# Performance work log

Measured on AMD Instinct MI355X. Metric: run time of the kernel, lower is better.

Reference implementation:

```python
import jax, jax.numpy as jnp
import numpy as np

N_NODES = 40000
N_EDGES = 640000
C = 128        # in_channels == hidden_channels
H = 8          # heads
D = C // H     # head dim = 16
L = 2          # num HGTConv layers
OUT = 64       # final fc out_channels


def _segment_softmax(logits, seg, num_segments):
    # logits: [E, H], seg: [E] destination ids
    m = jax.ops.segment_max(logits, seg, num_segments=num_segments)
    m = jnp.where(jnp.isfinite(m), m, 0.0)  # empty segments -> 0
    e = jnp.exp(logits - m[seg])
    s = jax.ops.segment_sum(e, seg, num_segments=num_segments)
    return e / (s[seg] + 1e-16)


def setup_inputs() -> dict:
    key = jax.random.key(0)
    ks = jax.random.split(key, 20)
    p = lambda k, shape, s=0.05: (jax.random.normal(k, shape, jnp.float32) * s)
    x = jax.random.normal(ks[0], (N_NODES, C), jnp.float32)
    edge_index = jax.random.randint(ks[1], (2, N_EDGES), 0, N_NODES, jnp.int64)
    return {
        "x": x,
        "edge_index": edge_index,
        # per-layer stacked params (all layers have C->C dims)
        "Wk": p(ks[2], (L, C, C)), "bk": jnp.zeros((L, C), jnp.float32),
        "Wq": p(ks[3], (L, C, C)), "bq": jnp.zeros((L, C), jnp.float32),
        "Wv": p(ks[4], (L, C, C)), "bv": jnp.zeros((L, C), jnp.float32),
        "a_rel": p(ks[5], (L, H, D, D), 0.1),  # relation key transform
        "m_rel": p(ks[6], (L, H, D, D), 0.1),  # relation message transform
        "p_rel": jnp.ones((L, H), jnp.float32),  # relation prior per head
        "skip": jnp.ones((L,), jnp.float32),      # skip gate logits
        "aW": p(ks[7], (L, C, C)), "ab": jnp.zeros((L, C), jnp.float32),
        "fcW": p(ks[8], (C, OUT)), "fcb": jnp.zeros((OUT,), jnp.float32),
    }


def reference(x, edge_index, Wk, bk, Wq, bq, Wv, bv, a_rel, m_rel, p_rel, skip,
              aW, ab, fcW, fcb):
    src, dst = edge_index[0], edge_index[1]
    n = x.shape[0]
    n_layers, heads, d = a_rel.shape[0], a_rel.shape[1], a_rel.shape[2]
    inv_sqrt_d = 1.0 / np.sqrt(d).astype(np.float32)

    h = x
    for l in range(n_layers):
        k = (h @ Wk[l] + bk[l]).reshape(n, heads, d)
        q = (h @ Wq[l] + bq[l]).reshape(n, heads, d)
        v = (h @ Wv[l] + bv[l]).reshape(n, heads, d)
        # relation-specific transforms applied at node level (single edge type)
        k2 = jnp.einsum('nhd,hde->nhe', k, a_rel[l])
        v2 = jnp.einsum('nhd,hde->nhe', v, m_rel[l])
        # per-edge attention logits [E, H]
        logits = jnp.sum(q[dst] * k2[src], axis=-1) * p_rel[l] * inv_sqrt_d
        alpha = _segment_softmax(logits, dst, n)                 # [E, H]
        msg = v2[src] * alpha[:, :, None]                        # [E, H, D]
        agg = jax.ops.segment_sum(msg, dst, num_segments=n)      # [N, H, D]
        agg = agg.reshape(n, heads * d)
        a = jax.nn.gelu(agg) @ aW[l] + ab[l]
        beta = jax.nn.sigmoid(skip[l])
        h = beta * a + (1.0 - beta) * h     # HGT skip (dims match)
        h = jax.nn.relu(h)                  # model-level relu
    return h @ fcW + fcb
```

## Files before the change

kernel.cpp:

```cpp
#include <hip/hip_runtime.h>
#include <hip/hip_bf16.h>
#include <math.h>

#define NN 40000
#define NE 640000

typedef __attribute__((ext_vector_type(8))) short short8;
typedef __attribute__((ext_vector_type(8))) unsigned short u16x8;
typedef __attribute__((ext_vector_type(4))) float f32x4;
typedef __attribute__((ext_vector_type(2))) float f32v2;
typedef _Float16 h16x2 __attribute__((ext_vector_type(2)));

#define WBLOCKS 547
#define GBLOCKS 625
#define NCO 157
#define P1B 160
#define EPB 4000
#define BCAP 5120

#if __has_builtin(__builtin_amdgcn_cvt_pk_f32_fp8) && __has_builtin(__builtin_amdgcn_cvt_pk_fp8_f32)
#define HAS_FP8CVT 1
#else
#define HAS_FP8CVT 0
#endif

__device__ __forceinline__ float fast_exp2(float x) {
#if __has_builtin(__builtin_amdgcn_exp2f)
    return __builtin_amdgcn_exp2f(x);
#else
    return exp2f(x);
#endif
}

__device__ __forceinline__ float gelu_tanh(float x) {
    float x3 = x * x * x;
    float u = 0.7978845608028654f * (x + 0.044715f * x3);
    float t = 1.0f - 2.0f / (1.0f + fast_exp2(2.885390081777927f * u));
    return 0.5f * x * (1.0f + t);
}

__device__ __forceinline__ unsigned short f2bf(float v) {
    __hip_bfloat16 h = __float2bfloat16(v);
    return *reinterpret_cast<unsigned short*>(&h);
}

__device__ __forceinline__ unsigned short f2h(float v) {
    union { _Float16 h; unsigned short u; } c;
    c.h = (_Float16)v;
    return c.u;
}

__device__ __forceinline__ float bf2f(unsigned short u) {
    union { unsigned int i; float f; } c;
    c.i = ((unsigned int)u) << 16;
    return c.f;
}

#if HAS_FP8CVT
__device__ __forceinline__ unsigned int f32x4_to_fp8(float a, float b, float c, float d) {
    int r = 0;
    r = __builtin_amdgcn_cvt_pk_fp8_f32(a, b, r, false);
    r = __builtin_amdgcn_cvt_pk_fp8_f32(c, d, r, true);
    return (unsigned int)r;
}
__device__ __forceinline__ void fp8x4_to_f32(unsigned int w, float* o) {
    f32v2 lo = __builtin_amdgcn_cvt_pk_f32_fp8((int)w, false);
    f32v2 hi = __builtin_amdgcn_cvt_pk_f32_fp8((int)w, true);
    o[0] = lo[0]; o[1] = lo[1]; o[2] = hi[0]; o[3] = hi[1];
}
#else
__device__ __forceinline__ unsigned char f2fp8_sw(float x) {
    union { float f; unsigned u; } c; c.f = x;
    unsigned sgn = (c.u >> 31) << 7;
    c.u &= 0x7fffffffu;
    if (!(c.f < 464.f)) return (unsigned char)(sgn | 0x7e);
    if (c.f < 0.0009765625f) return (unsigned char)sgn;
    if (c.f < 0.015625f) {
        int q = (int)rintf(c.f * 512.f);
        if (q > 7) return (unsigned char)(sgn | 0x08);
        return (unsigned char)(sgn | q);
    }
    unsigned u = c.u;
    unsigned lsb = (u >> 20) & 1;
    u += 0x7ffffu + lsb;
    int e8 = (int)(u >> 23) - 127 + 7;
    if (e8 > 15) return (unsigned char)(sgn | 0x7e);
    unsigned m = (u >> 20) & 7;
    return (unsigned char)(sgn | (e8 << 3) | m);
}
__device__ __forceinline__ float fp8_to_f32_sw(unsigned char b) {
    int e = (b >> 3) & 15, m = b & 7;
    float v = (e == 0) ? ldexpf((float)m, -9) : ldexpf(8.0f + (float)m, e - 10);
    return (b & 0x80) ? -v : v;
}
__device__ __forceinline__ unsigned int f32x4_to_fp8(float a, float b, float c, float d) {
    return (unsigned int)f2fp8_sw(a) | ((unsigned int)f2fp8_sw(b) << 8) |
           ((unsigned int)f2fp8_sw(c) << 16) | ((unsigned int)f2fp8_sw(d) << 24);
}
__device__ __forceinline__ void fp8x4_to_f32(unsigned int w, float* o) {
    o[0] = fp8_to_f32_sw((unsigned char)(w & 0xff));
    o[1] = fp8_to_f32_sw((unsigned char)((w >> 8) & 0xff));
    o[2] = fp8_to_f32_sw((unsigned char)((w >> 16) & 0xff));
    o[3] = fp8_to_f32_sw((unsigned char)((w >> 24) & 0xff));
}
#endif

union kv8 { u16x8 u; h16x2 p[4]; _Float16 h[8]; };
union frag8 { short8 s; unsigned short u[8]; u16x8 v; };

__global__ __launch_bounds__(256) void prep_kernel(
    const float* __restrict__ Wq, const float* __restrict__ bq,
    const float* __restrict__ Wk, const float* __restrict__ bk,
    const float* __restrict__ a_rel,
    const float* __restrict__ Wv, const float* __restrict__ bv,
    const float* __restrict__ m_rel,
    const float* __restrict__ p_rel,
    const float* __restrict__ aW, const float* __restrict__ fcW,
    unsigned short* __restrict__ BfT, float* __restrict__ biasf,
    unsigned short* __restrict__ aWT, unsigned short* __restrict__ fcWT,
    const int* __restrict__ eidx, int* __restrict__ gcur, int* __restrict__ ebuk)
{
    if (blockIdx.x < P1B) {
        __shared__ int cnt[NCO];
        __shared__ int cur[NCO];
        int b = blockIdx.x;
        int t = threadIdx.x;
        if (t < NCO) cnt[t] = 0;
        __syncthreads();
        int bs = b * EPB;
        for (int e = bs + t; e < bs + EPB; e += 256)
            atomicAdd(&cnt[eidx[NE + e] >> 8], 1);
        __syncthreads();
        if (t < NCO) cur[t] = atomicAdd(&gcur[t], cnt[t]);
        __syncthreads();
        for (int e = bs + t; e < bs + EPB; e += 256) {
            int s = eidx[e];
            int d = eidx[NE + e];
            int cb = d >> 8;
            int pos = atomicAdd(&cur[cb], 1);
            ebuk[cb * BCAP + pos] = ((d & 255) << 16) | s;
        }
        return;
    }
    int idx = (blockIdx.x - P1B) * 256 + threadIdx.x;
    if (idx < 2 * 129 * 384) {
        int l = idx / (129 * 384);
        int j = idx - l * (129 * 384);
        int r = j / 384;
        int col = j - r * 384;
        const float* Wq_l = Wq + l * 16384;
        const float* Wk_l = Wk + l * 16384;
        const float* Wv_l = Wv + l * 16384;
        const float* ar_l = a_rel + l * 2048;
        const float* mr_l = m_rel + l * 2048;
        float val;
        if (col < 128) {
            val = (r < 128) ? Wq_l[r * 128 + col] : bq[l * 128 + col];
        } else if (col < 256) {
            int cc = col - 128; int h = cc >> 4; int eo = cc & 15;
            float scale = p_rel[l * 8 + h] * 0.25f * 1.4426950408889634f;
            float s = 0.f;
            #pragma unroll
            for (int d = 0; d < 16; ++d) {
                float w = (r < 128) ? Wk_l[r * 128 + h * 16 + d] : bk[l * 128 + h * 16 + d];
                s += w * ar_l[h * 256 + d * 16 + eo];
            }
            val = s * scale;
        } else {
            int cc = col - 256; int h = cc >> 4; int eo = cc & 15;
            float s = 0.f;
            #pragma unroll
            for (int d = 0; d < 16; ++d) {
                float w = (r < 128) ? Wv_l[r * 128 + h * 16 + d] : bv[l * 128 + h * 16 + d];
                s += w * mr_l[h * 256 + d * 16 + eo];
            }
            val = s;
        }
        if (r < 128) BfT[(size_t)l * 49152 + (size_t)col * 128 + r] = f2bf(val);
        else         biasf[l * 384 + col] = val;
    } else if (idx < 2 * 129 * 384 + 2 * 16384) {
        int i = idx - 2 * 129 * 384;
        int l = i >> 14; int j = i & 16383;
        int r = j >> 7, c = j & 127;
        aWT[(size_t)l * 16384 + (size_t)c * 128 + r] = f2bf(aW[(size_t)l * 16384 + r * 128 + c]);
    } else {
        int i = idx - (2 * 129 * 384 + 2 * 16384);
        int c = i >> 7, r = i & 127;
        fcWT[(size_t)c * 128 + r] = f2bf(fcW[(size_t)r * 64 + c]);
    }
}

__global__ __launch_bounds__(256) void qkv0_p3_kernel(
    const float* __restrict__ Af, const unsigned short* __restrict__ BT,
    const float* __restrict__ bias,
    unsigned short* __restrict__ qb, unsigned char* __restrict__ kvb,
    const int* __restrict__ gcnt, const int* __restrict__ ebuk,
    int* __restrict__ deg, int* __restrict__ offs, int* __restrict__ srcSorted)
{
    if (blockIdx.x >= GBLOCKS) {
        __shared__ int hist[256], loffs[256], cur[256];
        int c = blockIdx.x - GBLOCKS;
        int t = threadIdx.x;
        int base = c * BCAP;
        int end = base + gcnt[c];
        hist[t] = 0;
        __syncthreads();
        for (int i = base + t; i < end; i += 256)
            atomicAdd(&hist[ebuk[i] >> 16], 1);
        __syncthreads();
        int v = hist[t];
        loffs[t] = v;
        __syncthreads();
        #pragma unroll
        for (int off = 1; off < 256; off <<= 1) {
            int u = (t >= off) ? loffs[t - off] : 0;
            __syncthreads();
            loffs[t] += u;
            __syncthreads();
        }
        int excl = loffs[t] - v;
        int n = c * 256 + t;
        if (n < NN) { deg[n] = v; offs[n] = base + excl; }
        cur[t] = excl;
        __syncthreads();
        for (int i = base + t; i < end; i += 256) {
            int p = ebuk[i];
            int pos = atomicAdd(&cur[p >> 16], 1);
            srcSorted[base + pos] = p & 0xffff;
        }
        return;
    }
    __shared__ unsigned short Bs[64][136];
    int t = threadIdx.x;
    int row0 = blockIdx.x * 64;
    int w = t >> 6;
    int lr = t & 15;
    int quad = (t & 63) >> 4;
    int row = row0 + w * 16 + lr;

    frag8 af[4];
    {
        const float* ap = Af + (size_t)row * 128 + quad * 8;
        #pragma unroll
        for (int kc = 0; kc < 4; ++kc) {
            float4 a0 = *(const float4*)(ap + kc * 32);
            float4 a1 = *(const float4*)(ap + kc * 32 + 4);
            af[kc].u[0] = f2bf(a0.x); af[kc].u[1] = f2bf(a0.y);
            af[kc].u[2] = f2bf(a0.z); af[kc].u[3] = f2bf(a0.w);
            af[kc].u[4] = f2bf(a1.x); af[kc].u[5] = f2bf(a1.y);
            af[kc].u[6] = f2bf(a1.z); af[kc].u[7] = f2bf(a1.w);
        }
    }

    #pragma unroll
    for (int ct = 0; ct < 6; ++ct) {
        if (ct) __syncthreads();
        #pragma unroll
        for (int i = 0; i < 4; ++i) {
            int idx = t + i * 256;
            int r = idx >> 4;
            int c8 = (idx & 15) * 8;
            *(u16x8*)(&Bs[r][c8]) = *(const u16x8*)(BT + (size_t)(ct * 64 + r) * 128 + c8);
        }
        __syncthreads();
        f32x4 acc[4] = {{0.f,0.f,0.f,0.f},{0.f,0.f,0.f,0.f},
                        {0.f,0.f,0.f,0.f},{0.f,0.f,0.f,0.f}};
        #pragma unroll
        for (int kc = 0; kc < 4; ++kc) {
            #pragma unroll
            for (int n4 = 0; n4 < 4; ++n4) {
                short8 bfr = *(const short8*)(&Bs[n4 * 16 + lr][kc * 32 + quad * 8]);
                acc[n4] = __builtin_amdgcn_mfma_f32_16x16x32_bf16(bfr, af[kc].s, acc[n4], 0, 0, 0);
            }
        }
        if (ct < 2) {
            unsigned short* dst = qb + (size_t)row * 128 + ct * 64;
            #pragma unroll
            for (int n4 = 0; n4 < 4; ++n4) {
                int colb = n4 * 16 + quad * 4;
                float4 bv = *(const float4*)(bias + ct * 64 + colb);
                ushort4 o;
                o.x = f2h(acc[n4][0] + bv.x);
                o.y = f2h(acc[n4][1] + bv.y);
                o.z = f2h(acc[n4][2] + bv.z);
                o.w = f2h(acc[n4][3] + bv.w);
                *(ushort4*)(dst + colb) = o;
            }
        } else {
            unsigned char* dst = kvb + (size_t)row * 256 + (ct - 2) * 64;
            #pragma unroll
            for (int n4 = 0; n4 < 4; ++n4) {
                int colb = n4 * 16 + quad * 4;
                float4 bv = *(const float4*)(bias + ct * 64 + colb);
                *(unsigned int*)(dst + colb) = f32x4_to_fp8(
                    acc[n4][0] + bv.x, acc[n4][1] + bv.y,
                    acc[n4][2] + bv.z, acc[n4][3] + bv.w);
            }
        }
    }
}

template <int HPFMT, int P2>
__global__ __launch_bounds__(256) void fused_kernel(
    const unsigned short* __restrict__ aggb,
    const unsigned short* __restrict__ aWT, const float* __restrict__ ab,
    const float* __restrict__ skip_p,
    const float* __restrict__ HprevF, const unsigned short* __restrict__ HprevB,
    unsigned short* __restrict__ hb_out,
    const unsigned short* __restrict__ W2T, const float* __restrict__ bias2,
    unsigned short* __restrict__ qb, unsigned char* __restrict__ kvb,
    float* __restrict__ outF)
{
    __shared__ unsigned short As[64][136];
    __shared__ unsigned short Bs[64][136];
    int t = threadIdx.x;
    int row0 = blockIdx.x * 64;
    int w = t >> 6;
    int lr = t & 15;
    int quad = (t & 63) >> 4;
    int row = row0 + w * 16 + lr;

    frag8 agf[4];
    {
        const unsigned short* ap = aggb + (size_t)row * 128 + quad * 8;
        #pragma unroll
        for (int kc = 0; kc < 4; ++kc) {
            u16x8 u = *(const u16x8*)(ap + kc * 32);
            #pragma unroll
            for (int j = 0; j < 8; ++j) agf[kc].u[j] = f2bf(gelu_tanh(bf2f(u[j])));
        }
    }

    float sv = skip_p[0];
    float beta = 1.f / (1.f + expf(-sv));
    float omb = 1.f - beta;

    f32x4 hacc[2][4];
    #pragma unroll
    for (int ct = 0; ct < 2; ++ct) {
        if (ct) __syncthreads();
        #pragma unroll
        for (int i = 0; i < 4; ++i) {
            int idx = t + i * 256;
            int r = idx >> 4;
            int c8 = (idx & 15) * 8;
            *(u16x8*)(&Bs[r][c8]) = *(const u16x8*)(aWT + (size_t)(ct * 64 + r) * 128 + c8);
        }
        __syncthreads();
        #pragma unroll
        for (int n4 = 0; n4 < 4; ++n4) hacc[ct][n4] = (f32x4){0.f,0.f,0.f,0.f};
        #pragma unroll
        for (int kc = 0; kc < 4; ++kc) {
            #pragma unroll
            for (int n4 = 0; n4 < 4; ++n4) {
                short8 bfr = *(const short8*)(&Bs[n4 * 16 + lr][kc * 32 + quad * 8]);
                hacc[ct][n4] = __builtin_amdgcn_mfma_f32_16x16x32_bf16(bfr, agf[kc].s, hacc[ct][n4], 0, 0, 0);
            }
        }
    }

    #pragma unroll
    for (int ct = 0; ct < 2; ++ct) {
        #pragma unroll
        for (int n4 = 0; n4 < 4; ++n4) {
            int colb = ct * 64 + n4 * 16 + quad * 4;
            float4 bv = *(const float4*)(ab + colb);
            float hp[4];
            if (HPFMT == 0) {
                float4 h4 = *(const float4*)(HprevF + (size_t)row * 128 + colb);
                hp[0] = h4.x; hp[1] = h4.y; hp[2] = h4.z; hp[3] = h4.w;
            } else {
                ushort4 h4 = *(const ushort4*)(HprevB + (size_t)row * 128 + colb);
                hp[0] = bf2f(h4.x); hp[1] = bf2f(h4.y); hp[2] = bf2f(h4.z); hp[3] = bf2f(h4.w);
            }
            ushort4 o;
            o.x = f2bf(fmaxf(beta * (hacc[ct][n4][0] + bv.x) + omb * hp[0], 0.f));
            o.y = f2bf(fmaxf(beta * (hacc[ct][n4][1] + bv.y) + omb * hp[1], 0.f));
            o.z = f2bf(fmaxf(beta * (hacc[ct][n4][2] + bv.z) + omb * hp[2], 0.f));
            o.w = f2bf(fmaxf(beta * (hacc[ct][n4][3] + bv.w) + omb * hp[3], 0.f));
            *(ushort4*)(&As[w * 16 + lr][colb]) = o;
            if (P2 == 0) *(ushort4*)(hb_out + (size_t)row * 128 + colb) = o;
        }
    }
    __syncthreads();

    if (P2 == 0) {
        #pragma unroll
        for (int ct = 0; ct < 6; ++ct) {
            if (ct) __syncthreads();
            #pragma unroll
            for (int i = 0; i < 4; ++i) {
                int idx = t + i * 256;
                int r = idx >> 4;
                int c8 = (idx & 15) * 8;
                *(u16x8*)(&Bs[r][c8]) = *(const u16x8*)(W2T + (size_t)(ct * 64 + r) * 128 + c8);
            }
            __syncthreads();
            f32x4 acc[4] = {{0.f,0.f,0.f,0.f},{0.f,0.f,0.f,0.f},
                            {0.f,0.f,0.f,0.f},{0.f,0.f,0.f,0.f}};
            #pragma unroll
            for (int kc = 0; kc < 4; ++kc) {
                short8 afr = *(const short8*)(&As[w * 16 + lr][kc * 32 + quad * 8]);
                #pragma unroll
                for (int n4 = 0; n4 < 4; ++n4) {
                    short8 bfr = *(const short8*)(&Bs[n4 * 16 + lr][kc * 32 + quad * 8]);
                    acc[n4] = __builtin_amdgcn_mfma_f32_16x16x32_bf16(bfr, afr, acc[n4], 0, 0, 0);
                }
            }
            if (ct < 2) {
                unsigned short* dst = qb + (size_t)row * 128 + ct * 64;
                #pragma unroll
                for (int n4 = 0; n4 < 4; ++n4) {
                    int colb = n4 * 16 + quad * 4;
                    float4 bv = *(const float4*)(bias2 + ct * 64 + colb);
                    ushort4 o;
                    o.x = f2h(acc[n4][0] + bv.x);
                    o.y = f2h(acc[n4][1] + bv.y);
                    o.z = f2h(acc[n4][2] + bv.z);
                    o.w = f2h(acc[n4][3] + bv.w);
                    *(ushort4*)(dst + colb) = o;
                }
            } else {
                unsigned char* dst = kvb + (size_t)row * 256 + (ct - 2) * 64;
                #pragma unroll
                for (int n4 = 0; n4 < 4; ++n4) {
                    int colb = n4 * 16 + quad * 4;
                    float4 bv = *(const float4*)(bias2 + ct * 64 + colb);
                    *(unsigned int*)(dst + colb) = f32x4_to_fp8(
                        acc[n4][0] + bv.x, acc[n4][1] + bv.y,
                        acc[n4][2] + bv.z, acc[n4][3] + bv.w);
                }
            }
        }
    } else {
        #pragma unroll
        for (int i = 0; i < 4; ++i) {
            int idx = t + i * 256;
            int r = idx >> 4;
            int c8 = (idx & 15) * 8;
            *(u16x8*)(&Bs[r][c8]) = *(const u16x8*)(W2T + (size_t)r * 128 + c8);
        }
        __syncthreads();
        f32x4 acc[4] = {{0.f,0.f,0.f,0.f},{0.f,0.f,0.f,0.f},
                        {0.f,0.f,0.f,0.f},{0.f,0.f,0.f,0.f}};
        #pragma unroll
        for (int kc = 0; kc < 4; ++kc) {
            short8 afr = *(const short8*)(&As[w * 16 + lr][kc * 32 + quad * 8]);
            #pragma unroll
            for (int n4 = 0; n4 < 4; ++n4) {
                short8 bfr = *(const short8*)(&Bs[n4 * 16 + lr][kc * 32 + quad * 8]);
                acc[n4] = __builtin_amdgcn_mfma_f32_16x16x32_bf16(bfr, afr, acc[n4], 0, 0, 0);
            }
        }
        #pragma unroll
        for (int n4 = 0; n4 < 4; ++n4) {
            int colb = n4 * 16 + quad * 4;
            float4 bv = *(const float4*)(bias2 + colb);
            float4 o;
            o.x = acc[n4][0] + bv.x;
            o.y = acc[n4][1] + bv.y;
            o.z = acc[n4][2] + bv.z;
            o.w = acc[n4][3] + bv.w;
            *(float4*)(outF + (size_t)row * 64 + colb) = o;
        }
    }
}

__global__ __launch_bounds__(256) void aggregate_kernel(
    const unsigned short* __restrict__ qb, const unsigned char* __restrict__ kvb,
    const int* __restrict__ deg, const int* __restrict__ offs,
    const int* __restrict__ srcSorted, unsigned short* __restrict__ aggb)
{
    int n = (blockIdx.x * 256 + threadIdx.x) >> 6;
    int lane = threadIdx.x & 63;
    int es = lane >> 3;
    int h = lane & 7;

    float qf[16];
    {
        kv8 a, b;
        a.u = *(const u16x8*)(qb + (size_t)n * 128 + h * 16);
        b.u = *(const u16x8*)(qb + (size_t)n * 128 + h * 16 + 8);
        #pragma unroll
        for (int j = 0; j < 8; ++j) { qf[j] = (float)a.h[j]; qf[8 + j] = (float)b.h[j]; }
    }
    float acc[16];
    #pragma unroll
    for (int j = 0; j < 16; ++j) acc[j] = 0.f;
    float den = 0.f;

    int start = offs[n];
    int d = deg[n];
    if (d > 0) {
        int ng = (d + 7) >> 3;
        int lastIdx = start + d - 1;

        int4 kA, vA, kB, vB;
        {
            int i0 = start + es; if (i0 > lastIdx) i0 = lastIdx;
            const unsigned char* p = kvb + (size_t)srcSorted[i0] * 256 + h * 16;
            kA = *(const int4*)p;
            vA = *(const int4*)(p + 128);
        }
        kB = kA; vB = vA;
        if (ng > 1) {
            int i1 = start + 8 + es; if (i1 > lastIdx) i1 = lastIdx;
            const unsigned char* p = kvb + (size_t)srcSorted[i1] * 256 + h * 16;
            kB = *(const int4*)p;
            vB = *(const int4*)(p + 128);
        }

        for (int g = 0; g < ng; ++g) {
            int4 kC = kA, vC = vA;
            if (g + 2 < ng) {
                int ni = start + (g + 2) * 8 + es; if (ni > lastIdx) ni = lastIdx;
                const unsigned char* p = kvb + (size_t)srcSorted[ni] * 256 + h * 16;
                kC = *(const int4*)p;
                vC = *(const int4*)(p + 128);
            }
            float pdot = 0.f;
            {
                float kf[16];
                fp8x4_to_f32((unsigned int)kA.x, kf);
                fp8x4_to_f32((unsigned int)kA.y, kf + 4);
                fp8x4_to_f32((unsigned int)kA.z, kf + 8);
                fp8x4_to_f32((unsigned int)kA.w, kf + 12);
                #pragma unroll
                for (int j = 0; j < 16; ++j) pdot = fmaf(kf[j], qf[j], pdot);
            }
            float ev = (g * 8 + es < d) ? fast_exp2(pdot) : 0.f;
            den += ev;
            {
                float vf[16];
                fp8x4_to_f32((unsigned int)vA.x, vf);
                fp8x4_to_f32((unsigned int)vA.y, vf + 4);
                fp8x4_to_f32((unsigned int)vA.z, vf + 8);
                fp8x4_to_f32((unsigned int)vA.w, vf + 12);
                #pragma unroll
                for (int j = 0; j < 16; ++j) acc[j] = fmaf(vf[j], ev, acc[j]);
            }
            kA = kB; vA = vB;
            kB = kC; vB = vC;
        }
    }
    #pragma unroll
    for (int m = 8; m < 64; m <<= 1) {
        den += __shfl_xor(den, m, 64);
        #pragma unroll
        for (int j = 0; j < 16; ++j) acc[j] += __shfl_xor(acc[j], m, 64);
    }
    if (es == 0) {
        float w = 1.f / (den + 1e-16f);
        u16x8 o0, o1;
        #pragma unroll
        for (int j = 0; j < 8; ++j) {
            o0[j] = f2bf(acc[j] * w);
            o1[j] = f2bf(acc[j + 8] * w);
        }
        *(u16x8*)(aggb + (size_t)n * 128 + h * 16) = o0;
        *(u16x8*)(aggb + (size_t)n * 128 + h * 16 + 8) = o1;
    }
}

extern "C" void kernel_launch(void* const* d_in, const int* in_sizes, int n_in,
                              void* d_out, int out_size, void* d_ws, size_t ws_size,
                              hipStream_t stream) {
    const float* x     = (const float*)d_in[0];
    const int*   eidx  = (const int*)d_in[1];
    const float* Wk    = (const float*)d_in[2];
    const float* bk    = (const float*)d_in[3];
    const float* Wq    = (const float*)d_in[4];
    const float* bq    = (const float*)d_in[5];
    const float* Wv    = (const float*)d_in[6];
    const float* bv    = (const float*)d_in[7];
    const float* a_rel = (const float*)d_in[8];
    const float* m_rel = (const float*)d_in[9];
    const float* p_rel = (const float*)d_in[10];
    const float* skip  = (const float*)d_in[11];
    const float* aW    = (const float*)d_in[12];
    const float* ab    = (const float*)d_in[13];
    const float* fcW   = (const float*)d_in[14];
    const float* fcb   = (const float*)d_in[15];
    float* out = (float*)d_out;

    float* biasf = (float*)d_ws;
    unsigned short* hb   = (unsigned short*)(biasf + 768);
    unsigned short* qb   = hb + (size_t)NN * 128;
    unsigned char*  kvb  = (unsigned char*)(qb + (size_t)NN * 128);
    unsigned short* aggb = (unsigned short*)(kvb + (size_t)NN * 256);
    unsigned short* BfT  = aggb + (size_t)NN * 128;
    unsigned short* aWT  = BfT + 2 * 384 * 128;
    unsigned short* fcWT = aWT + 2 * 128 * 128;
    int* deg       = (int*)(fcWT + 64 * 128);
    int* offs      = deg + NN;
    int* gcur      = offs + NN;
    int* ebuk      = gcur + 160;
    int* srcSorted = ebuk + NCO * BCAP;

    hipMemsetAsync(gcur, 0, NCO * sizeof(int), stream);

    prep_kernel<<<P1B + WBLOCKS, 256, 0, stream>>>(
        Wq, bq, Wk, bk, a_rel, Wv, bv, m_rel, p_rel, aW, fcW,
        BfT, biasf, aWT, fcWT, eidx, gcur, ebuk);

    qkv0_p3_kernel<<<GBLOCKS + NCO, 256, 0, stream>>>(
        x, BfT, biasf, qb, kvb, gcur, ebuk, deg, offs, srcSorted);
    aggregate_kernel<<<NN / 4, 256, 0, stream>>>(qb, kvb, deg, offs, srcSorted, aggb);

    fused_kernel<0, 0><<<GBLOCKS, 256, 0, stream>>>(
        aggb, aWT, ab, skip, x, nullptr, hb,
        BfT + 49152, biasf + 384, qb, kvb, nullptr);
    aggregate_kernel<<<NN / 4, 256, 0, stream>>>(qb, kvb, deg, offs, srcSorted, aggb);

    fused_kernel<1, 2><<<GBLOCKS, 256, 0, stream>>>(
        aggb, aWT + 16384, ab + 128, skip + 1, nullptr, hb, nullptr,
        fcWT, fcb, nullptr, nullptr, out);
}
```

Measured before the change: 240.1 us.

## Fuse edge aggregation into the per-layer GEMM kernel via shared memory

```diff
diff --git a/kernel.cpp b/kernel.cpp
--- a/kernel.cpp
+++ b/kernel.cpp
@@ -195,7 +195,7 @@
     const float* __restrict__ bias,
     unsigned short* __restrict__ qb, unsigned char* __restrict__ kvb,
     const int* __restrict__ gcnt, const int* __restrict__ ebuk,
-    int* __restrict__ deg, int* __restrict__ offs, int* __restrict__ srcSorted)
+    int* __restrict__ podeg, int* __restrict__ srcSorted)
 {
     if (blockIdx.x >= GBLOCKS) {
         __shared__ int hist[256], loffs[256], cur[256];
@@ -220,7 +220,7 @@
         }
         int excl = loffs[t] - v;
         int n = c * 256 + t;
-        if (n < NN) { deg[n] = v; offs[n] = base + excl; }
+        if (n < NN) podeg[n] = (base + excl) | (v << 20);
         cur[t] = excl;
         __syncthreads();
         for (int i = base + t; i < end; i += 256) {
@@ -301,14 +301,15 @@
 }
 
 template <int HPFMT, int P2>
-__global__ __launch_bounds__(256) void fused_kernel(
-    const unsigned short* __restrict__ aggb,
+__global__ __launch_bounds__(256) void merged_kernel(
+    const unsigned short* __restrict__ qb, const unsigned char* __restrict__ kvb,
+    const int* __restrict__ podeg, const int* __restrict__ srcSorted,
     const unsigned short* __restrict__ aWT, const float* __restrict__ ab,
     const float* __restrict__ skip_p,
     const float* __restrict__ HprevF, const unsigned short* __restrict__ HprevB,
     unsigned short* __restrict__ hb_out,
     const unsigned short* __restrict__ W2T, const float* __restrict__ bias2,
-    unsigned short* __restrict__ qb, unsigned char* __restrict__ kvb,
+    unsigned short* __restrict__ qb_out, unsigned char* __restrict__ kvb_out,
     float* __restrict__ outF)
 {
     __shared__ unsigned short As[64][136];
@@ -316,19 +317,110 @@
     int t = threadIdx.x;
     int row0 = blockIdx.x * 64;
     int w = t >> 6;
+    int lane = t & 63;
+    int es = lane >> 3;
+    int h = lane & 7;
+
+    for (int it = 0; it < 16; ++it) {
+        int n = row0 + w * 16 + it;
+        float qf[16];
+        {
+            kv8 a, b;
+            a.u = *(const u16x8*)(qb + (size_t)n * 128 + h * 16);
+            b.u = *(const u16x8*)(qb + (size_t)n * 128 + h * 16 + 8);
+            #pragma unroll
+            for (int j = 0; j < 8; ++j) { qf[j] = (float)a.h[j]; qf[8 + j] = (float)b.h[j]; }
+        }
+        float acc[16];
+        #pragma unroll
+        for (int j = 0; j < 16; ++j) acc[j] = 0.f;
+        float den = 0.f;
+
+        int pd = podeg[n];
+        int start = pd & 0xFFFFF;
+        int d = ((unsigned)pd) >> 20;
+        if (d > 0) {
+            int ng = (d + 7) >> 3;
+            int lastIdx = start + d - 1;
+
+            int4 kA, vA, kB, vB;
+            {
+                int i0 = start + es; if (i0 > lastIdx) i0 = lastIdx;
+                const unsigned char* p = kvb + (size_t)srcSorted[i0] * 256 + h * 16;
+                kA = *(const int4*)p;
+                vA = *(const int4*)(p + 128);
+            }
+            kB = kA; vB = vA;
+            if (ng > 1) {
+                int i1 = start + 8 + es; if (i1 > lastIdx) i1 = lastIdx;
+                const unsigned char* p = kvb + (size_t)srcSorted[i1] * 256 + h * 16;
+                kB = *(const int4*)p;
+                vB = *(const int4*)(p + 128);
+            }
+
+            for (int g = 0; g < ng; ++g) {
+                int4 kC = kA, vC = vA;
+                if (g + 2 < ng) {
+                    int ni = start + (g + 2) * 8 + es; if (ni > lastIdx) ni = lastIdx;
+                    const unsigned char* p = kvb + (size_t)srcSorted[ni] * 256 + h * 16;
+                    kC = *(const int4*)p;
+                    vC = *(const int4*)(p + 128);
+                }
+                float pdot = 0.f;
+                {
+                    float kf[16];
+                    fp8x4_to_f32((unsigned int)kA.x, kf);
+                    fp8x4_to_f32((unsigned int)kA.y, kf + 4);
+                    fp8x4_to_f32((unsigned int)kA.z, kf + 8);
+                    fp8x4_to_f32((unsigned int)kA.w, kf + 12);
+                    #pragma unroll
+                    for (int j = 0; j < 16; ++j) pdot = fmaf(kf[j], qf[j], pdot);
+                }
+                float ev = (g * 8 + es < d) ? fast_exp2(pdot) : 0.f;
+                den += ev;
+                {
+                    float vf[16];
+                    fp8x4_to_f32((unsigned int)vA.x, vf);
+                    fp8x4_to_f32((unsigned int)vA.y, vf + 4);
+                    fp8x4_to_f32((unsigned int)vA.z, vf + 8);
+                    fp8x4_to_f32((unsigned int)vA.w, vf + 12);
+                    #pragma unroll
+                    for (int j = 0; j < 16; ++j) acc[j] = fmaf(vf[j], ev, acc[j]);
+                }
+                kA = kB; vA = vB;
+                kB = kC; vB = vC;
+            }
+        }
+        #pragma unroll
+        for (int m = 8; m < 64; m <<= 1) {
+            den += __shfl_xor(den, m, 64);
+            #pragma unroll
+            for (int j = 0; j < 16; ++j) acc[j] += __shfl_xor(acc[j], m, 64);
+        }
+        if (es == 0) {
+            float wd = 1.f / (den + 1e-16f);
+            u16x8 o0, o1;
+            #pragma unroll
+            for (int j = 0; j < 8; ++j) {
+                o0[j] = f2bf(acc[j] * wd);
+                o1[j] = f2bf(acc[j + 8] * wd);
+            }
+            *(u16x8*)(&As[w * 16 + it][h * 16]) = o0;
+            *(u16x8*)(&As[w * 16 + it][h * 16 + 8]) = o1;
+        }
+    }
+    __syncthreads();
+
     int lr = t & 15;
     int quad = (t & 63) >> 4;
     int row = row0 + w * 16 + lr;
 
     frag8 agf[4];
-    {
-        const unsigned short* ap = aggb + (size_t)row * 128 + quad * 8;
-        #pragma unroll
-        for (int kc = 0; kc < 4; ++kc) {
-            u16x8 u = *(const u16x8*)(ap + kc * 32);
-            #pragma unroll
-            for (int j = 0; j < 8; ++j) agf[kc].u[j] = f2bf(gelu_tanh(bf2f(u[j])));
-        }
+    #pragma unroll
+    for (int kc = 0; kc < 4; ++kc) {
+        u16x8 u = *(const u16x8*)(&As[w * 16 + lr][kc * 32 + quad * 8]);
+        #pragma unroll
+        for (int j = 0; j < 8; ++j) agf[kc].u[j] = f2bf(gelu_tanh(bf2f(u[j])));
     }
 
     float sv = skip_p[0];
@@ -338,7 +430,7 @@
     f32x4 hacc[2][4];
     #pragma unroll
     for (int ct = 0; ct < 2; ++ct) {
-        if (ct) __syncthreads();
+        __syncthreads();
         #pragma unroll
         for (int i = 0; i < 4; ++i) {
             int idx = t + i * 256;
@@ -358,6 +450,7 @@
             }
         }
     }
+    __syncthreads();
 
     #pragma unroll
     for (int ct = 0; ct < 2; ++ct) {
@@ -408,7 +501,7 @@
                 }
             }
             if (ct < 2) {
-                unsigned short* dst = qb + (size_t)row * 128 + ct * 64;
+                unsigned short* dst = qb_out + (size_t)row * 128 + ct * 64;
                 #pragma unroll
                 for (int n4 = 0; n4 < 4; ++n4) {
                     int colb = n4 * 16 + quad * 4;
@@ -421,7 +514,7 @@
                     *(ushort4*)(dst + colb) = o;
                 }
             } else {
-                unsigned char* dst = kvb + (size_t)row * 256 + (ct - 2) * 64;
+                unsigned char* dst = kvb_out + (size_t)row * 256 + (ct - 2) * 64;
                 #pragma unroll
                 for (int n4 = 0; n4 < 4; ++n4) {
                     int colb = n4 * 16 + quad * 4;
@@ -463,102 +556,6 @@
             o.w = acc[n4][3] + bv.w;
             *(float4*)(outF + (size_t)row * 64 + colb) = o;
         }
-    }
-}
-
-__global__ __launch_bounds__(256) void aggregate_kernel(
-    const unsigned short* __restrict__ qb, const unsigned char* __restrict__ kvb,
-    const int* __restrict__ deg, const int* __restrict__ offs,
-    const int* __restrict__ srcSorted, unsigned short* __restrict__ aggb)
-{
-    int n = (blockIdx.x * 256 + threadIdx.x) >> 6;
-    int lane = threadIdx.x & 63;
-    int es = lane >> 3;
-    int h = lane & 7;
-
-    float qf[16];
-    {
-        kv8 a, b;
-        a.u = *(const u16x8*)(qb + (size_t)n * 128 + h * 16);
-        b.u = *(const u16x8*)(qb + (size_t)n * 128 + h * 16 + 8);
-        #pragma unroll
-        for (int j = 0; j < 8; ++j) { qf[j] = (float)a.h[j]; qf[8 + j] = (float)b.h[j]; }
-    }
-    float acc[16];
-    #pragma unroll
-    for (int j = 0; j < 16; ++j) acc[j] = 0.f;
-    float den = 0.f;
-
-    int start = offs[n];
-    int d = deg[n];
-    if (d > 0) {
-        int ng = (d + 7) >> 3;
-        int lastIdx = start + d - 1;
-
-        int4 kA, vA, kB, vB;
-        {
-            int i0 = start + es; if (i0 > lastIdx) i0 = lastIdx;
-            const unsigned char* p = kvb + (size_t)srcSorted[i0] * 256 + h * 16;
-            kA = *(const int4*)p;
-            vA = *(const int4*)(p + 128);
-        }
-        kB = kA; vB = vA;
-        if (ng > 1) {
-            int i1 = start + 8 + es; if (i1 > lastIdx) i1 = lastIdx;
-            const unsigned char* p = kvb + (size_t)srcSorted[i1] * 256 + h * 16;
-            kB = *(const int4*)p;
-            vB = *(const int4*)(p + 128);
-        }
-
-        for (int g = 0; g < ng; ++g) {
-            int4 kC = kA, vC = vA;
-            if (g + 2 < ng) {
-                int ni = start + (g + 2) * 8 + es; if (ni > lastIdx) ni = lastIdx;
-                const unsigned char* p = kvb + (size_t)srcSorted[ni] * 256 + h * 16;
-                kC = *(const int4*)p;
-                vC = *(const int4*)(p + 128);
-            }
-            float pdot = 0.f;
-            {
-                float kf[16];
-                fp8x4_to_f32((unsigned int)kA.x, kf);
-                fp8x4_to_f32((unsigned int)kA.y, kf + 4);
-                fp8x4_to_f32((unsigned int)kA.z, kf + 8);
-                fp8x4_to_f32((unsigned int)kA.w, kf + 12);
-                #pragma unroll
-                for (int j = 0; j < 16; ++j) pdot = fmaf(kf[j], qf[j], pdot);
-            }
-            float ev = (g * 8 + es < d) ? fast_exp2(pdot) : 0.f;
-            den += ev;
-            {
-                float vf[16];
-                fp8x4_to_f32((unsigned int)vA.x, vf);
-                fp8x4_to_f32((unsigned int)vA.y, vf + 4);
-                fp8x4_to_f32((unsigned int)vA.z, vf + 8);
-                fp8x4_to_f32((unsigned int)vA.w, vf + 12);
-                #pragma unroll
-                for (int j = 0; j < 16; ++j) acc[j] = fmaf(vf[j], ev, acc[j]);
-            }
-            kA = kB; vA = vB;
-            kB = kC; vB = vC;
-        }
-    }
-    #pragma unroll
-    for (int m = 8; m < 64; m <<= 1) {
-        den += __shfl_xor(den, m, 64);
-        #pragma unroll
-        for (int j = 0; j < 16; ++j) acc[j] += __shfl_xor(acc[j], m, 64);
-    }
-    if (es == 0) {
-        float w = 1.f / (den + 1e-16f);
-        u16x8 o0, o1;
-        #pragma unroll
-        for (int j = 0; j < 8; ++j) {
-            o0[j] = f2bf(acc[j] * w);
-            o1[j] = f2bf(acc[j + 8] * w);
-        }
-        *(u16x8*)(aggb + (size_t)n * 128 + h * 16) = o0;
-        *(u16x8*)(aggb + (size_t)n * 128 + h * 16 + 8) = o1;
     }
 }
 
@@ -585,15 +582,15 @@
 
     float* biasf = (float*)d_ws;
     unsigned short* hb   = (unsigned short*)(biasf + 768);
-    unsigned short* qb   = hb + (size_t)NN * 128;
-    unsigned char*  kvb  = (unsigned char*)(qb + (size_t)NN * 128);
-    unsigned short* aggb = (unsigned short*)(kvb + (size_t)NN * 256);
-    unsigned short* BfT  = aggb + (size_t)NN * 128;
+    unsigned short* qb0  = hb + (size_t)NN * 128;
+    unsigned char*  kvb0 = (unsigned char*)(qb0 + (size_t)NN * 128);
+    unsigned short* qb1  = (unsigned short*)(kvb0 + (size_t)NN * 256);
+    unsigned char*  kvb1 = (unsigned char*)(qb1 + (size_t)NN * 128);
+    unsigned short* BfT  = (unsigned short*)(kvb1 + (size_t)NN * 256);
     unsigned short* aWT  = BfT + 2 * 384 * 128;
     unsigned short* fcWT = aWT + 2 * 128 * 128;
-    int* deg       = (int*)(fcWT + 64 * 128);
-    int* offs      = deg + NN;
-    int* gcur      = offs + NN;
+    int* podeg     = (int*)(fcWT + 64 * 128);
+    int* gcur      = podeg + NN;
     int* ebuk      = gcur + 160;
     int* srcSorted = ebuk + NCO * BCAP;
 
@@ -604,15 +601,13 @@
         BfT, biasf, aWT, fcWT, eidx, gcur, ebuk);
 
     qkv0_p3_kernel<<<GBLOCKS + NCO, 256, 0, stream>>>(
-        x, BfT, biasf, qb, kvb, gcur, ebuk, deg, offs, srcSorted);
-    aggregate_kernel<<<NN / 4, 256, 0, stream>>>(qb, kvb, deg, offs, srcSorted, aggb);
-
-    fused_kernel<0, 0><<<GBLOCKS, 256, 0, stream>>>(
-        aggb, aWT, ab, skip, x, nullptr, hb,
-        BfT + 49152, biasf + 384, qb, kvb, nullptr);
-    aggregate_kernel<<<NN / 4, 256, 0, stream>>>(qb, kvb, deg, offs, srcSorted, aggb);
-
-    fused_kernel<1, 2><<<GBLOCKS, 256, 0, stream>>>(
-        aggb, aWT + 16384, ab + 128, skip + 1, nullptr, hb, nullptr,
+        x, BfT, biasf, qb0, kvb0, gcur, ebuk, podeg, srcSorted);
+
+    merged_kernel<0, 0><<<GBLOCKS, 256, 0, stream>>>(
+        qb0, kvb0, podeg, srcSorted, aWT, ab, skip, x, nullptr, hb,
+        BfT + 49152, biasf + 384, qb1, kvb1, nullptr);
+
+    merged_kernel<1, 2><<<GBLOCKS, 256, 0, stream>>>(
+        qb1, kvb1, podeg, srcSorted, aWT + 16384, ab + 128, skip + 1, nullptr, hb, nullptr,
         fcWT, fcb, nullptr, nullptr, out);
 }
```

Result: slower. 276.1 us (+15.0%).

## Prefetch next weight tile into registers during MFMA and pack offset/degree

Applied to the files above, without the earlier changes.

```diff
diff --git a/kernel.cpp b/kernel.cpp
--- a/kernel.cpp
+++ b/kernel.cpp
@@ -195,7 +195,7 @@
     const float* __restrict__ bias,
     unsigned short* __restrict__ qb, unsigned char* __restrict__ kvb,
     const int* __restrict__ gcnt, const int* __restrict__ ebuk,
-    int* __restrict__ deg, int* __restrict__ offs, int* __restrict__ srcSorted)
+    int* __restrict__ podeg, int* __restrict__ srcSorted)
 {
     if (blockIdx.x >= GBLOCKS) {
         __shared__ int hist[256], loffs[256], cur[256];
@@ -220,7 +220,7 @@
         }
         int excl = loffs[t] - v;
         int n = c * 256 + t;
-        if (n < NN) { deg[n] = v; offs[n] = base + excl; }
+        if (n < NN) podeg[n] = (base + excl) | (v << 20);
         cur[t] = excl;
         __syncthreads();
         for (int i = base + t; i < end; i += 256) {
@@ -237,6 +237,8 @@
     int lr = t & 15;
     int quad = (t & 63) >> 4;
     int row = row0 + w * 16 + lr;
+    int sr = t >> 4;
+    int sc8 = (t & 15) * 8;
 
     frag8 af[4];
     {
@@ -252,17 +254,22 @@
         }
     }
 
+    u16x8 stg[4];
+    #pragma unroll
+    for (int i = 0; i < 4; ++i)
+        stg[i] = *(const u16x8*)(BT + (size_t)(sr + i * 16) * 128 + sc8);
+    #pragma unroll
+    for (int i = 0; i < 4; ++i)
+        *(u16x8*)(&Bs[sr + i * 16][sc8]) = stg[i];
+    __syncthreads();
+
     #pragma unroll
     for (int ct = 0; ct < 6; ++ct) {
-        if (ct) __syncthreads();
-        #pragma unroll
-        for (int i = 0; i < 4; ++i) {
-            int idx = t + i * 256;
-            int r = idx >> 4;
-            int c8 = (idx & 15) * 8;
-            *(u16x8*)(&Bs[r][c8]) = *(const u16x8*)(BT + (size_t)(ct * 64 + r) * 128 + c8);
-        }
-        __syncthreads();
+        if (ct < 5) {
+            #pragma unroll
+            for (int i = 0; i < 4; ++i)
+                stg[i] = *(const u16x8*)(BT + (size_t)((ct + 1) * 64 + sr + i * 16) * 128 + sc8);
+        }
         f32x4 acc[4] = {{0.f,0.f,0.f,0.f},{0.f,0.f,0.f,0.f},
                         {0.f,0.f,0.f,0.f},{0.f,0.f,0.f,0.f}};
         #pragma unroll
@@ -296,6 +303,13 @@
                     acc[n4][0] + bv.x, acc[n4][1] + bv.y,
                     acc[n4][2] + bv.z, acc[n4][3] + bv.w);
             }
+        }
+        __syncthreads();
+        if (ct < 5) {
+            #pragma unroll
+            for (int i = 0; i < 4; ++i)
+                *(u16x8*)(&Bs[sr + i * 16][sc8]) = stg[i];
+            __syncthreads();
         }
     }
 }
@@ -319,6 +333,8 @@
     int lr = t & 15;
     int quad = (t & 63) >> 4;
     int row = row0 + w * 16 + lr;
+    int sr = t >> 4;
+    int sc8 = (t & 15) * 8;
 
     frag8 agf[4];
     {
@@ -335,27 +351,45 @@
     float beta = 1.f / (1.f + expf(-sv));
     float omb = 1.f - beta;
 
+    u16x8 stg[4];
+    #pragma unroll
+    for (int i = 0; i < 4; ++i)
+        stg[i] = *(const u16x8*)(aWT + (size_t)(sr + i * 16) * 128 + sc8);
+    #pragma unroll
+    for (int i = 0; i < 4; ++i)
+        *(u16x8*)(&Bs[sr + i * 16][sc8]) = stg[i];
+    __syncthreads();
+
     f32x4 hacc[2][4];
     #pragma unroll
-    for (int ct = 0; ct < 2; ++ct) {
-        if (ct) __syncthreads();
-        #pragma unroll
-        for (int i = 0; i < 4; ++i) {
-            int idx = t + i * 256;
-            int r = idx >> 4;
-            int c8 = (idx & 15) * 8;
-            *(u16x8*)(&Bs[r][c8]) = *(const u16x8*)(aWT + (size_t)(ct * 64 + r) * 128 + c8);
-        }
-        __syncthreads();
-        #pragma unroll
-        for (int n4 = 0; n4 < 4; ++n4) hacc[ct][n4] = (f32x4){0.f,0.f,0.f,0.f};
-        #pragma unroll
-        for (int kc = 0; kc < 4; ++kc) {
-            #pragma unroll
-            for (int n4 = 0; n4 < 4; ++n4) {
-                short8 bfr = *(const short8*)(&Bs[n4 * 16 + lr][kc * 32 + quad * 8]);
-                hacc[ct][n4] = __builtin_amdgcn_mfma_f32_16x16x32_bf16(bfr, agf[kc].s, hacc[ct][n4], 0, 0, 0);
-            }
+    for (int i = 0; i < 4; ++i)
+        stg[i] = *(const u16x8*)(aWT + (size_t)(64 + sr + i * 16) * 128 + sc8);
+    #pragma unroll
+    for (int n4 = 0; n4 < 4; ++n4) hacc[0][n4] = (f32x4){0.f,0.f,0.f,0.f};
+    #pragma unroll
+    for (int kc = 0; kc < 4; ++kc) {
+        #pragma unroll
+        for (int n4 = 0; n4 < 4; ++n4) {
+            short8 bfr = *(const short8*)(&Bs[n4 * 16 + lr][kc * 32 + quad * 8]);
+            hacc[0][n4] = __builtin_amdgcn_mfma_f32_16x16x32_bf16(bfr, agf[kc].s, hacc[0][n4], 0, 0, 0);
+        }
+    }
+    __syncthreads();
+    #pragma unroll
+    for (int i = 0; i < 4; ++i)
+        *(u16x8*)(&Bs[sr + i * 16][sc8]) = stg[i];
+    __syncthreads();
+    #pragma unroll
+    for (int i = 0; i < 4; ++i)
+        stg[i] = *(const u16x8*)(W2T + (size_t)(sr + i * 16) * 128 + sc8);
+    #pragma unroll
+    for (int n4 = 0; n4 < 4; ++n4) hacc[1][n4] = (f32x4){0.f,0.f,0.f,0.f};
+    #pragma unroll
+    for (int kc = 0; kc < 4; ++kc) {
+        #pragma unroll
+        for (int n4 = 0; n4 < 4; ++n4) {
+            short8 bfr = *(const short8*)(&Bs[n4 * 16 + lr][kc * 32 + quad * 8]);
+            hacc[1][n4] = __builtin_amdgcn_mfma_f32_16x16x32_bf16(bfr, agf[kc].s, hacc[1][n4], 0, 0, 0);
         }
     }
 
@@ -383,19 +417,19 @@
         }
     }
     __syncthreads();
+    #pragma unroll
+    for (int i = 0; i < 4; ++i)
+        *(u16x8*)(&Bs[sr + i * 16][sc8]) = stg[i];
+    __syncthreads();
 
     if (P2 == 0) {
         #pragma unroll
         for (int ct = 0; ct < 6; ++ct) {
-            if (ct) __syncthreads();
-            #pragma unroll
-            for (int i = 0; i < 4; ++i) {
-                int idx = t + i * 256;
-                int r = idx >> 4;
-                int c8 = (idx & 15) * 8;
-                *(u16x8*)(&Bs[r][c8]) = *(const u16x8*)(W2T + (size_t)(ct * 64 + r) * 128 + c8);
-            }
-            __syncthreads();
+            if (ct < 5) {
+                #pragma unroll
+                for (int i = 0; i < 4; ++i)
+                    stg[i] = *(const u16x8*)(W2T + (size_t)((ct + 1) * 64 + sr + i * 16) * 128 + sc8);
+            }
             f32x4 acc[4] = {{0.f,0.f,0.f,0.f},{0.f,0.f,0.f,0.f},
                             {0.f,0.f,0.f,0.f},{0.f,0.f,0.f,0.f}};
             #pragma unroll
@@ -431,16 +465,15 @@
                         acc[n4][2] + bv.z, acc[n4][3] + bv.w);
                 }
             }
+            __syncthreads();
+            if (ct < 5) {
+                #pragma unroll
+                for (int i = 0; i < 4; ++i)
+                    *(u16x8*)(&Bs[sr + i * 16][sc8]) = stg[i];
+                __syncthreads();
+            }
         }
     } else {
-        #pragma unroll
-        for (int i = 0; i < 4; ++i) {
-            int idx = t + i * 256;
-            int r = idx >> 4;
-            int c8 = (idx & 15) * 8;
-            *(u16x8*)(&Bs[r][c8]) = *(const u16x8*)(W2T + (size_t)r * 128 + c8);
-        }
-        __syncthreads();
         f32x4 acc[4] = {{0.f,0.f,0.f,0.f},{0.f,0.f,0.f,0.f},
                         {0.f,0.f,0.f,0.f},{0.f,0.f,0.f,0.f}};
         #pragma unroll
@@ -468,7 +501,7 @@
 
 __global__ __launch_bounds__(256) void aggregate_kernel(
     const unsigned short* __restrict__ qb, const unsigned char* __restrict__ kvb,
-    const int* __restrict__ deg, const int* __restrict__ offs,
+    const int* __restrict__ podeg,
     const int* __restrict__ srcSorted, unsigned short* __restrict__ aggb)
 {
     int n = (blockIdx.x * 256 + threadIdx.x) >> 6;
@@ -489,8 +522,9 @@
     for (int j = 0; j < 16; ++j) acc[j] = 0.f;
     float den = 0.f;
 
-    int start = offs[n];
-    int d = deg[n];
+    int pd = podeg[n];
+    int start = pd & 0xFFFFF;
+    int d = ((unsigned)pd) >> 20;
     if (d > 0) {
         int ng = (d + 7) >> 3;
         int lastIdx = start + d - 1;
@@ -591,9 +625,8 @@
     unsigned short* BfT  = aggb + (size_t)NN * 128;
     unsigned short* aWT  = BfT + 2 * 384 * 128;
     unsigned short* fcWT = aWT + 2 * 128 * 128;
-    int* deg       = (int*)(fcWT + 64 * 128);
-    int* offs      = deg + NN;
-    int* gcur      = offs + NN;
+    int* podeg     = (int*)(fcWT + 64 * 128);
+    int* gcur      = podeg + NN;
     int* ebuk      = gcur + 160;
     int* srcSorted = ebuk + NCO * BCAP;
 
@@ -604,13 +637,15 @@
         BfT, biasf, aWT, fcWT, eidx, gcur, ebuk);
 
     qkv0_p3_kernel<<<GBLOCKS + NCO, 256, 0, stream>>>(
-        x, BfT, biasf, qb, kvb, gcur, ebuk, deg, offs, srcSorted);
-    aggregate_kernel<<<NN / 4, 256, 0, stream>>>(qb, kvb, deg, offs, srcSorted, aggb);
+        x, BfT, biasf, qb, kvb, gcur, ebuk, podeg, srcSorted);
+
+    aggregate_kernel<<<NN / 4, 256, 0, stream>>>(qb, kvb, podeg, srcSorted, aggb);
 
     fused_kernel<0, 0><<<GBLOCKS, 256, 0, stream>>>(
         aggb, aWT, ab, skip, x, nullptr, hb,
         BfT + 49152, biasf + 384, qb, kvb, nullptr);
-    aggregate_kernel<<<NN / 4, 256, 0, stream>>>(qb, kvb, deg, offs, srcSorted, aggb);
+
+    aggregate_kernel<<<NN / 4, 256, 0, stream>>>(qb, kvb, podeg, srcSorted, aggb);
 
     fused_kernel<1, 2><<<GBLOCKS, 256, 0, stream>>>(
         aggb, aWT + 16384, ab + 128, skip + 1, nullptr, hb, nullptr,
```

Measured after the change: 242.5 us. About the same (+1.0%).
